# Optimization experiments

Measured on AMD Instinct MI355X. Metric: run time of the kernel, lower is better.

Reference implementation:

```python
import jax, jax.numpy as jnp
import numpy as np

B, P, D = 256, 128, 768        # batch, property slots per sample, encoder hidden dim
E = 64                          # num_properties (number of adapter heads)
H = 256                         # adapter_hidden_dim
H2 = H // 2
O = 2                           # output_dim
LN_EPS = 1e-5
RES_W_ADPT, RES_W_BASE = 0.7, 0.3


def setup_inputs() -> dict:
    key = jax.random.key(0)
    ks = jax.random.split(key, 12)
    hidden_states = jax.random.normal(ks[0], (B, P, D), dtype=jnp.float32)
    base_output = jax.random.normal(ks[1], (B, P, O), dtype=jnp.float32)
    properties = jax.random.randint(ks[2], (B, P), 0, E, dtype=jnp.int64)
    mask = (jax.random.uniform(ks[3], (B, P)) > 0.1).astype(jnp.float32)
    # Stacked per-head adapter parameters (LayerNorm + 3 Linears per head)
    ln_g = jnp.ones((E, D), dtype=jnp.float32)
    ln_b = jnp.zeros((E, D), dtype=jnp.float32)
    W1 = jax.random.normal(ks[4], (E, D, H), dtype=jnp.float32) * (1.0 / np.sqrt(D))
    b1 = jnp.zeros((E, H), dtype=jnp.float32)
    W2 = jax.random.normal(ks[5], (E, H, H2), dtype=jnp.float32) * (1.0 / np.sqrt(H))
    b2 = jnp.zeros((E, H2), dtype=jnp.float32)
    W3 = jax.random.normal(ks[6], (E, H2, O), dtype=jnp.float32) * 0.01  # init std=0.01 per source
    b3 = jnp.zeros((E, O), dtype=jnp.float32)
    return {
        "hidden_states": hidden_states, "base_output": base_output,
        "properties": properties, "mask": mask,
        "ln_g": ln_g, "ln_b": ln_b, "W1": W1, "b1": b1,
        "W2": W2, "b2": b2, "W3": W3, "b3": b3,
    }


def reference(hidden_states, base_output, properties, mask,
              ln_g, ln_b, W1, b1, W2, b2, W3, b3):
    b, p, d = hidden_states.shape
    o = W3.shape[-1]
    x = hidden_states.reshape(-1, d)                        # [N, D]
    # LayerNorm statistics are head-independent; only gamma/beta differ per head
    mu = jnp.mean(x, axis=-1, keepdims=True)
    var = jnp.mean((x - mu) ** 2, axis=-1, keepdims=True)
    xhat = (x - mu) * jax.lax.rsqrt(var + LN_EPS)           # [N, D]
    flat_p = properties.reshape(-1)                         # [N]
    flat_m = mask.reshape(-1)                               # [N]

    def body(acc, inp):
        idx, g, bt, w1, bb1, w2, bb2, w3, bb3 = inp
        h = jax.nn.relu((xhat * g + bt) @ w1 + bb1)         # [N, H]  (dropout = identity in eval)
        h = jax.nn.relu(h @ w2 + bb2)                       # [N, H2]
        out = h @ w3 + bb3                                  # [N, O]
        sel = (flat_p == idx) & (flat_m > 0)
        return jnp.where(sel[:, None], out, acc), None

    e = W1.shape[0]
    acc0 = jnp.zeros((b * p, o), dtype=x.dtype)
    acc, _ = jax.lax.scan(
        body, acc0,
        (jnp.arange(e), ln_g, ln_b, W1, b1, W2, b2, W3, b3))
    out = acc.reshape(b, p, o)
    out = RES_W_ADPT * out + RES_W_BASE * base_output       # use_residual=True
    return out * mask[..., None]
```

## Files before the change

kernel.cpp:

```cpp
#include <hip/hip_runtime.h>
#include <stdint.h>

typedef unsigned short u16;
typedef unsigned int   u32;

#define NTOK   32768
#define GD     768
#define GH     256
#define GH2    128
#define GE     64

typedef __bf16 bf16x8 __attribute__((ext_vector_type(8)));
typedef float  f32x4  __attribute__((ext_vector_type(4)));
union Frag { uint4 u; bf16x8 b; };

__device__ __forceinline__ float bf2f(u16 h) {
  union { u32 u; float f; } v; v.u = ((u32)h) << 16; return v.f;
}
__device__ __forceinline__ u16 f2bf(float f) {
  union { float f; u32 u; } v; v.f = f;
  u32 r = (v.u + 0x7fffu + ((v.u >> 16) & 1u)) >> 16;
  return (u16)r;
}

__device__ __forceinline__ void bar_lds() {
  asm volatile("s_waitcnt lgkmcnt(0)" ::: "memory");
  __builtin_amdgcn_sched_barrier(0);
  __builtin_amdgcn_s_barrier();
  __builtin_amdgcn_sched_barrier(0);
}

__device__ __forceinline__ int getProp(const int* p32, int t, int is64) {
  return is64 ? p32[2 * t] : p32[t];
}

static const size_t OFF_W1T  = 0;
static const size_t OFF_W2T  = 25165824;
static const size_t OFF_TOK  = 29360128;
static const size_t OFF_META = 29491200;

__global__ void setup_kernel(const int* __restrict__ prop, const float* __restrict__ mask,
                             u32* __restrict__ outz, int* __restrict__ counts2d,
                             int* __restrict__ cursors_p, int* __restrict__ flagp) {
  __shared__ int h[GE];
  __shared__ int vOr;
  const int b = blockIdx.x;
  const int tid = threadIdx.x;
  outz[b * 512 + tid] = 0u;
  outz[b * 512 + 256 + tid] = 0u;
  if (b < 4) cursors_p[b * 256 + tid] = 0;
  if (tid < GE) h[tid] = 0;
  if (tid == 0) vOr = 0;
  __syncthreads();
  int v = prop[2 * tid + 1] | prop[2 * (tid + 256) + 1];
  if (v) atomicOr(&vOr, 1);
  __syncthreads();
  const int is64 = (vOr == 0) ? 1 : 0;
  if (b == 0 && tid == 0) *flagp = is64;
  const int t = b * 256 + tid;
  if (mask[t] > 0.f) atomicAdd(&h[getProp(prop, t, is64)], 1);
  __syncthreads();
  if (tid < GE) counts2d[b * GE + tid] = h[tid];
}

__global__ void transpose_w1(const float* __restrict__ in, u16* __restrict__ out) {
  __shared__ u16 tl[64][260];
  const int bid = blockIdx.x;
  const int e  = bid / 12, r = bid % 12;
  const int d0 = (r / 4) * 256, h0 = (r % 4) * 64;
  const int tid = threadIdx.x;
  const size_t inMat = (size_t)e * GD * GH;
  const size_t outMat = (size_t)e * GH * GD;
  const int h_l = (tid & 15) * 4, d_l = tid >> 4;
#pragma unroll
  for (int dd = 0; dd < 16; ++dd) {
    const int d = d_l + dd * 16;
    float4 v = *(const float4*)(in + inMat + (size_t)(d0 + d) * GH + h0 + h_l);
    tl[h_l + 0][d] = f2bf(v.x);
    tl[h_l + 1][d] = f2bf(v.y);
    tl[h_l + 2][d] = f2bf(v.z);
    tl[h_l + 3][d] = f2bf(v.w);
  }
  __syncthreads();
  const int wv = tid >> 6, ln = tid & 63;
  const int d_glob = d0 + ln * 4;
  const size_t tbase = outMat + (size_t)(d_glob >> 5) * 8192 +
                       (size_t)((d_glob >> 3) & 3) * 2048 + (d_glob & 7);
#pragma unroll
  for (int hh = 0; hh < 16; ++hh) {
    const int h = wv * 16 + hh;
    *(uint2*)(out + tbase + (size_t)(h0 + h) * 8) = *(const uint2*)&tl[h][ln * 4];
  }
}

__global__ void transpose_w2(const float* __restrict__ in, u16* __restrict__ out) {
  __shared__ u16 tile[32][33];
  const int tilesPerMat = 32;
  const int e  = blockIdx.x / tilesPerMat;
  const int t  = blockIdx.x % tilesPerMat;
  const int tr = t / 4, tc = t % 4;
  const size_t mat = (size_t)e * GH * GH2;
  const int tx = threadIdx.x & 31, ty = threadIdx.x >> 5;
  const int r0 = tr * 32, c0 = tc * 32;
#pragma unroll
  for (int i = 0; i < 32; i += 8)
    tile[ty + i][tx] = f2bf(in[mat + (size_t)(r0 + ty + i) * GH2 + c0 + tx]);
  __syncthreads();
  const int k = r0 + tx;
  const size_t kbase = mat + (size_t)(k >> 5) * 4096 +
                       (size_t)((k >> 3) & 3) * 1024 + (k & 7);
#pragma unroll
  for (int i = 0; i < 32; i += 8)
    out[kbase + (size_t)(c0 + ty + i) * 8] = tile[tx][ty + i];
}

__global__ void scan_kernel(const int* __restrict__ counts2d, int* __restrict__ offsets,
                            int* __restrict__ tileHead, int* __restrict__ tileRow,
                            int* __restrict__ nTilesPtr) {
  __shared__ int part[4][GE];
  const int tid = threadIdx.x;
  const int e = tid & 63, q = tid >> 6;
  int c = 0;
  for (int b = q * 32; b < q * 32 + 32; ++b) c += counts2d[b * GE + e];
  part[q][e] = c;
  __syncthreads();
  if (tid < GE) {
    const int ct = part[0][e] + part[1][e] + part[2][e] + part[3][e];
    int inc = ct;
#pragma unroll
    for (int d = 1; d < 64; d <<= 1) { int n = __shfl_up(inc, d); if (e >= d) inc += n; }
    const int off = inc - ct;
    offsets[e] = off;
    if (e == 63) offsets[64] = inc;
    int ntile = (ct + 63) >> 6;
    int inct = ntile;
#pragma unroll
    for (int d = 1; d < 64; d <<= 1) { int n = __shfl_up(inct, d); if (e >= d) inct += n; }
    const int tb = inct - ntile;
    for (int j = 0; j < ntile; ++j) { tileHead[tb + j] = e; tileRow[tb + j] = off + j * 64; }
    if (e == 63) *nTilesPtr = inct;
  }
}

__global__ void scatter_kernel(const int* __restrict__ prop, const float* __restrict__ mask,
                               const int* __restrict__ offsets, int* __restrict__ cursors_p,
                               int* __restrict__ tokenIds, const int* __restrict__ flag) {
  __shared__ int h[GE];
  __shared__ int basebin[GE];
  const int tid = threadIdx.x;
  const int t = blockIdx.x * 256 + tid;
  if (tid < GE) h[tid] = 0;
  __syncthreads();
  int p = -1, rank = 0;
  if (mask[t] > 0.f) {
    p = getProp(prop, t, *flag);
    rank = atomicAdd(&h[p], 1);
  }
  __syncthreads();
  if (tid < GE && h[tid] > 0) basebin[tid] = atomicAdd(&cursors_p[tid * 16], h[tid]);
  __syncthreads();
  if (p >= 0) tokenIds[offsets[p] + basebin[p] + rank] = t;
}

__global__ __launch_bounds__(256, 2) void adapter_gemm(
    const float* __restrict__ hs, const u16* __restrict__ w1t, const u16* __restrict__ w2t,
    const float* __restrict__ lng, const float* __restrict__ lnb,
    const float* __restrict__ b1, const float* __restrict__ b2,
    const float* __restrict__ w3, const float* __restrict__ b3,
    const float* __restrict__ base, const float* __restrict__ mask,
    const int* __restrict__ tokenIds, const int* __restrict__ offsets,
    const int* __restrict__ tileHead, const int* __restrict__ tileRow,
    const int* __restrict__ nTilesPtr, float* __restrict__ outp) {
  __shared__ union LU {
    u16 A[3][2048];
    u16 h[17408];
  } uni;
  __shared__ float sBias1[256];
  __shared__ float sBias2[128];
  __shared__ float sW3[2][128];
  __shared__ float sB3[2];
  __shared__ int   sTok[64];
  __shared__ __align__(16) float sGam[GD];
  __shared__ __align__(16) float sBet[GD];
  __shared__ float sMu[64];
  __shared__ float sRstd[64];

  const int tid  = threadIdx.x;
  const int wv   = tid >> 6;
  const int l15  = tid & 15;
  const int quad = (tid & 63) >> 4;
  const f32x4 vzero = {0.f, 0.f, 0.f, 0.f};
  const int nt = *nTilesPtr;
  const int qq = nt >> 3, rr = nt & 7;

  for (int i = blockIdx.x; i < nt; i += gridDim.x) {
    const int x = i & 7, s = i >> 3;
    const int tile = (x < rr ? x * (qq + 1) : rr * (qq + 1) + (x - rr) * qq) + s;

    __syncthreads();
    const int e  = tileHead[tile];
    const int rs = tileRow[tile];
    const int nRows = min(64, offsets[e + 1] - rs);

    if (tid < 64) sTok[tid] = tokenIds[rs + min(tid, nRows - 1)];
    sBias1[tid] = b1[e * GH + tid];
    if (tid < 128) sBias2[tid] = b2[e * GH2 + tid];
    { const int k = tid >> 1, o = tid & 1; sW3[o][k] = w3[e * GH2 * 2 + k * 2 + o]; }
    if (tid < 2) sB3[tid] = b3[e * 2 + tid];
    __syncthreads();

    const u16* w1e = w1t + (size_t)e * GH * GD;
    const u16* w2e = w2t + (size_t)e * GH2 * GH;

    if (tid < 192) {
      *(float4*)&sGam[tid * 4] = *(const float4*)(lng + (size_t)e * GD + tid * 4);
      *(float4*)&sBet[tid * 4] = *(const float4*)(lnb + (size_t)e * GD + tid * 4);
    }

    const int r0  = tid >> 3;
    const int klo = (tid & 7) * 4;
    const int kgrp = klo >> 3, kin = klo & 7;
    const float* xA = hs + (size_t)sTok[r0] * GD + klo;
    const float* xB = hs + (size_t)sTok[r0 + 32] * GD + klo;

    Frag fbE[4], fbO[4];
#define LOAD_FB(DST, KT) do {                                                   \
    const u16* _g = w1e + (KT) * 8192 + quad * 2048;                            \
    DST[0].u = *(const uint4*)(_g + (size_t)(wv * 64 +  0 + l15) * 8);          \
    DST[1].u = *(const uint4*)(_g + (size_t)(wv * 64 + 16 + l15) * 8);          \
    DST[2].u = *(const uint4*)(_g + (size_t)(wv * 64 + 32 + l15) * 8);          \
    DST[3].u = *(const uint4*)(_g + (size_t)(wv * 64 + 48 + l15) * 8);          \
  } while (0)

#define ISSUE_PA(D, KT) do {                                                    \
    pA[D][0] = *(const float4*)(xA + (KT) * 32);                                \
    pA[D][1] = *(const float4*)(xB + (KT) * 32);                                \
  } while (0)

    float4 pA[3][2];
    ISSUE_PA(0, 0);
    ISSUE_PA(1, 1);
    ISSUE_PA(2, 2);
    LOAD_FB(fbE, 0);
    LOAD_FB(fbO, 1);
    __builtin_amdgcn_sched_barrier(0);

#pragma unroll 2
    for (int pass = 0; pass < 4; ++pass) {
      const int row = pass * 16 + (tid >> 4);
      const int l16 = tid & 15;
      const float* xp = hs + (size_t)sTok[row] * GD + l16 * 4;
      float sm = 0.f, sq = 0.f;
#pragma unroll
      for (int c = 0; c < 12; ++c) {
        float4 u = *(const float4*)(xp + c * 64);
        sm += u.x + u.y + u.z + u.w;
        sq += u.x*u.x + u.y*u.y + u.z*u.z + u.w*u.w;
      }
#pragma unroll
      for (int d = 1; d < 16; d <<= 1) { sm += __shfl_xor(sm, d); sq += __shfl_xor(sq, d); }
      if (l16 == 0) {
        const float mu = sm * (1.f / 768.f);
        sMu[row] = mu;
        sRstd[row] = rsqrtf(sq * (1.f / 768.f) - mu * mu + 1e-5f);
      }
    }
    bar_lds();

    const float muA = sMu[r0],      rsA = sRstd[r0];
    const float muB = sMu[r0 + 32], rsB = sRstd[r0 + 32];

#define XFORM_WRITE(PAR, D, K0) do {                                            \
    const float4 gv = *(const float4*)&sGam[(K0) + klo];                        \
    const float4 bv = *(const float4*)&sBet[(K0) + klo];                        \
    const float4 va = pA[D][0], vb = pA[D][1];                                  \
    uint2 oa, ob;                                                               \
    oa.x = (u32)f2bf((va.x - muA) * rsA * gv.x + bv.x)                          \
         | ((u32)f2bf((va.y - muA) * rsA * gv.y + bv.y) << 16);                 \
    oa.y = (u32)f2bf((va.z - muA) * rsA * gv.z + bv.z)                          \
         | ((u32)f2bf((va.w - muA) * rsA * gv.w + bv.w) << 16);                 \
    ob.x = (u32)f2bf((vb.x - muB) * rsB * gv.x + bv.x)                          \
         | ((u32)f2bf((vb.y - muB) * rsB * gv.y + bv.y) << 16);                 \
    ob.y = (u32)f2bf((vb.z - muB) * rsB * gv.z + bv.z)                          \
         | ((u32)f2bf((vb.w - muB) * rsB * gv.w + bv.w) << 16);                 \
    *(uint2*)&uni.A[PAR][kgrp * 512 + r0 * 8 + kin] = oa;                       \
    *(uint2*)&uni.A[PAR][kgrp * 512 + (r0 + 32) * 8 + kin] = ob;                \
  } while (0)

    XFORM_WRITE(0, 0, 0);
    XFORM_WRITE(1, 1, 32);
    bar_lds();

    f32x4 acc1[4][4];
#pragma unroll
    for (int f = 0; f < 4; ++f)
#pragma unroll
      for (int g = 0; g < 4; ++g) acc1[f][g] = vzero;

#pragma unroll
    for (int kt = 0; kt < 24; ++kt) {
      Frag fa[4];
#pragma unroll
      for (int f = 0; f < 4; ++f)
        fa[f].u = *(const uint4*)&uni.A[kt % 3][quad * 512 + (f * 16 + l15) * 8];
      if ((kt & 1) == 0) {
#pragma unroll
        for (int f = 0; f < 4; ++f)
#pragma unroll
          for (int g = 0; g < 4; ++g)
            acc1[f][g] = __builtin_amdgcn_mfma_f32_16x16x32_bf16(fa[f].b, fbE[g].b, acc1[f][g], 0, 0, 0);
        if (kt + 2 < 24) LOAD_FB(fbE, kt + 2);
      } else {
#pragma unroll
        for (int f = 0; f < 4; ++f)
#pragma unroll
          for (int g = 0; g < 4; ++g)
            acc1[f][g] = __builtin_amdgcn_mfma_f32_16x16x32_bf16(fa[f].b, fbO[g].b, acc1[f][g], 0, 0, 0);
        if (kt + 2 < 24) LOAD_FB(fbO, kt + 2);
      }
      if (kt + 2 < 24)
        XFORM_WRITE((kt + 2) % 3, (kt + 2) % 3, (kt + 2) * 32);
      if (kt + 3 < 24)
        ISSUE_PA((kt + 3) % 3, kt + 3);
      bar_lds();
    }
    bar_lds();

    Frag bW2[8][2];
#pragma unroll
    for (int kt = 0; kt < 8; ++kt)
#pragma unroll
      for (int g = 0; g < 2; ++g)
        bW2[kt][g].u = *(const uint4*)(w2e + kt * 4096 + quad * 1024 +
                                       (size_t)(wv * 32 + g * 16 + l15) * 8);

#pragma unroll
    for (int f = 0; f < 4; ++f)
#pragma unroll
      for (int g = 0; g < 4; ++g) {
        const int col = wv * 64 + g * 16 + l15;
        const float bias = sBias1[col];
#pragma unroll
        for (int r = 0; r < 4; ++r) {
          const int row = f * 16 + quad * 4 + r;
          uni.h[row * 264 + col] = f2bf(fmaxf(acc1[f][g][r] + bias, 0.f));
        }
      }
    bar_lds();

    f32x4 acc2[4][2];
#pragma unroll
    for (int f = 0; f < 4; ++f)
#pragma unroll
      for (int g = 0; g < 2; ++g) acc2[f][g] = vzero;

#pragma unroll
    for (int kt = 0; kt < 8; ++kt) {
      Frag fa2[4];
#pragma unroll
      for (int f = 0; f < 4; ++f)
        fa2[f].u = *(const uint4*)&uni.h[(f * 16 + l15) * 264 + kt * 32 + quad * 8];
#pragma unroll
      for (int f = 0; f < 4; ++f)
#pragma unroll
        for (int g = 0; g < 2; ++g)
          acc2[f][g] = __builtin_amdgcn_mfma_f32_16x16x32_bf16(fa2[f].b, bW2[kt][g].b, acc2[f][g], 0, 0, 0);
    }
    bar_lds();

#pragma unroll
    for (int f = 0; f < 4; ++f)
#pragma unroll
      for (int g = 0; g < 2; ++g) {
        const int col = wv * 32 + g * 16 + l15;
        const float bias = sBias2[col];
#pragma unroll
        for (int r = 0; r < 4; ++r) {
          const int row = f * 16 + quad * 4 + r;
          uni.h[row * 130 + col] = f2bf(fmaxf(acc2[f][g][r] + bias, 0.f));
        }
      }
    bar_lds();

    const int m = tid >> 1, o = tid & 1;
    if (m < nRows) {
      float a = sB3[o];
      const u16* h2row = &uni.h[m * 130];
#pragma unroll 16
      for (int k = 0; k < 128; ++k) a += bf2f(h2row[k]) * sW3[o][k];
      const int t = sTok[m];
      const float mk = mask[t];
      const float bs = base[t * 2 + o];
      outp[t * 2 + o] = (0.7f * a + 0.3f * bs) * mk;
    }
  }
#undef XFORM_WRITE
#undef ISSUE_PA
#undef LOAD_FB
}

extern "C" void kernel_launch(void* const* d_in, const int* in_sizes, int n_in,
                              void* d_out, int out_size, void* d_ws, size_t ws_size,
                              hipStream_t stream) {
  const float* hs   = (const float*)d_in[0];
  const float* base = (const float*)d_in[1];
  const int*   prop = (const int*)d_in[2];
  const float* mask = (const float*)d_in[3];
  const float* lng  = (const float*)d_in[4];
  const float* lnb  = (const float*)d_in[5];
  const float* W1   = (const float*)d_in[6];
  const float* b1   = (const float*)d_in[7];
  const float* W2   = (const float*)d_in[8];
  const float* b2   = (const float*)d_in[9];
  const float* W3   = (const float*)d_in[10];
  const float* b3   = (const float*)d_in[11];

  char* ws = (char*)d_ws;
  u16* w1t  = (u16*)(ws + OFF_W1T);
  u16* w2t  = (u16*)(ws + OFF_W2T);
  int* tok  = (int*)(ws + OFF_TOK);
  int* meta = (int*)(ws + OFF_META);
  int* counts2d  = meta;
  int* offsets   = meta + 8192;
  int* tileHead  = meta + 8320;
  int* tileRow   = meta + 9344;
  int* nTiles    = meta + 10368;
  int* propFlag  = meta + 10369;
  int* cursors_p = meta + 10432;

  setup_kernel<<<128, 256, 0, stream>>>(prop, mask, (u32*)d_out, counts2d,
                                        cursors_p, propFlag);
  transpose_w1<<<768, 256, 0, stream>>>(W1, w1t);
  transpose_w2<<<64 * 32, 256, 0, stream>>>(W2, w2t);
  scan_kernel<<<1, 256, 0, stream>>>(counts2d, offsets, tileHead, tileRow, nTiles);
  scatter_kernel<<<NTOK / 256, 256, 0, stream>>>(prop, mask, offsets, cursors_p, tok, propFlag);
  adapter_gemm<<<640, 256, 0, stream>>>(hs, w1t, w2t, lng, lnb, b1, b2, W3, b3,
                                        base, mask, tok, offsets, tileHead, tileRow,
                                        nTiles, (float*)d_out);
}
```

Baseline: 250.9 us.

## Fuse weight transposes, widen scan, quad-buffer A tile with fewer barriers

Merges the W1 and W2 bf16 transpose kernels into a single launch, and widens the count-reduction scan to 1024 threads. In the GEMM main loop, the A-tile LDS buffer grows from three to four slots so a barrier is needed only every other k-step. The W3 dot product also uses four independent accumulators. Together these aim to cut launch overhead and barrier stalls, at the cost of more LDS per block and more reliance on getting the buffer-reuse distance right.

```diff
diff --git a/kernel.cpp b/kernel.cpp
--- a/kernel.cpp
+++ b/kernel.cpp
@@ -63,69 +63,74 @@
   if (tid < GE) counts2d[b * GE + tid] = h[tid];
 }
 
-__global__ void transpose_w1(const float* __restrict__ in, u16* __restrict__ out) {
+__global__ void transpose_fused(const float* __restrict__ in1, u16* __restrict__ out1,
+                                const float* __restrict__ in2, u16* __restrict__ out2) {
   __shared__ u16 tl[64][260];
-  const int bid = blockIdx.x;
-  const int e  = bid / 12, r = bid % 12;
-  const int d0 = (r / 4) * 256, h0 = (r % 4) * 64;
   const int tid = threadIdx.x;
-  const size_t inMat = (size_t)e * GD * GH;
-  const size_t outMat = (size_t)e * GH * GD;
-  const int h_l = (tid & 15) * 4, d_l = tid >> 4;
-#pragma unroll
-  for (int dd = 0; dd < 16; ++dd) {
-    const int d = d_l + dd * 16;
-    float4 v = *(const float4*)(in + inMat + (size_t)(d0 + d) * GH + h0 + h_l);
-    tl[h_l + 0][d] = f2bf(v.x);
-    tl[h_l + 1][d] = f2bf(v.y);
-    tl[h_l + 2][d] = f2bf(v.z);
-    tl[h_l + 3][d] = f2bf(v.w);
+  if (blockIdx.x < 768) {
+    const int bid = blockIdx.x;
+    const int e  = bid / 12, r = bid % 12;
+    const int d0 = (r / 4) * 256, h0 = (r % 4) * 64;
+    const size_t inMat = (size_t)e * GD * GH;
+    const size_t outMat = (size_t)e * GH * GD;
+    const int h_l = (tid & 15) * 4, d_l = tid >> 4;
+#pragma unroll
+    for (int dd = 0; dd < 16; ++dd) {
+      const int d = d_l + dd * 16;
+      float4 v = *(const float4*)(in1 + inMat + (size_t)(d0 + d) * GH + h0 + h_l);
+      tl[h_l + 0][d] = f2bf(v.x);
+      tl[h_l + 1][d] = f2bf(v.y);
+      tl[h_l + 2][d] = f2bf(v.z);
+      tl[h_l + 3][d] = f2bf(v.w);
+    }
+    __syncthreads();
+    const int wv = tid >> 6, ln = tid & 63;
+    const int d_glob = d0 + ln * 4;
+    const size_t tbase = outMat + (size_t)(d_glob >> 5) * 8192 +
+                         (size_t)((d_glob >> 3) & 3) * 2048 + (d_glob & 7);
+#pragma unroll
+    for (int hh = 0; hh < 16; ++hh) {
+      const int h = wv * 16 + hh;
+      *(uint2*)(out1 + tbase + (size_t)(h0 + h) * 8) = *(const uint2*)&tl[h][ln * 4];
+    }
+  } else {
+    u16 (*tile)[33] = (u16(*)[33])tl;
+    const int bid = blockIdx.x - 768;
+    const int tilesPerMat = 32;
+    const int e  = bid / tilesPerMat;
+    const int t  = bid % tilesPerMat;
+    const int tr = t / 4, tc = t % 4;
+    const size_t mat = (size_t)e * GH * GH2;
+    const int tx = tid & 31, ty = tid >> 5;
+    const int r0 = tr * 32, c0 = tc * 32;
+#pragma unroll
+    for (int i = 0; i < 32; i += 8)
+      tile[ty + i][tx] = f2bf(in2[mat + (size_t)(r0 + ty + i) * GH2 + c0 + tx]);
+    __syncthreads();
+    const int k = r0 + tx;
+    const size_t kbase = mat + (size_t)(k >> 5) * 4096 +
+                         (size_t)((k >> 3) & 3) * 1024 + (k & 7);
+#pragma unroll
+    for (int i = 0; i < 32; i += 8)
+      out2[kbase + (size_t)(c0 + ty + i) * 8] = tile[tx][ty + i];
   }
-  __syncthreads();
-  const int wv = tid >> 6, ln = tid & 63;
-  const int d_glob = d0 + ln * 4;
-  const size_t tbase = outMat + (size_t)(d_glob >> 5) * 8192 +
-                       (size_t)((d_glob >> 3) & 3) * 2048 + (d_glob & 7);
-#pragma unroll
-  for (int hh = 0; hh < 16; ++hh) {
-    const int h = wv * 16 + hh;
-    *(uint2*)(out + tbase + (size_t)(h0 + h) * 8) = *(const uint2*)&tl[h][ln * 4];
-  }
-}
-
-__global__ void transpose_w2(const float* __restrict__ in, u16* __restrict__ out) {
-  __shared__ u16 tile[32][33];
-  const int tilesPerMat = 32;
-  const int e  = blockIdx.x / tilesPerMat;
-  const int t  = blockIdx.x % tilesPerMat;
-  const int tr = t / 4, tc = t % 4;
-  const size_t mat = (size_t)e * GH * GH2;
-  const int tx = threadIdx.x & 31, ty = threadIdx.x >> 5;
-  const int r0 = tr * 32, c0 = tc * 32;
-#pragma unroll
-  for (int i = 0; i < 32; i += 8)
-    tile[ty + i][tx] = f2bf(in[mat + (size_t)(r0 + ty + i) * GH2 + c0 + tx]);
-  __syncthreads();
-  const int k = r0 + tx;
-  const size_t kbase = mat + (size_t)(k >> 5) * 4096 +
-                       (size_t)((k >> 3) & 3) * 1024 + (k & 7);
-#pragma unroll
-  for (int i = 0; i < 32; i += 8)
-    out[kbase + (size_t)(c0 + ty + i) * 8] = tile[tx][ty + i];
 }
 
 __global__ void scan_kernel(const int* __restrict__ counts2d, int* __restrict__ offsets,
                             int* __restrict__ tileHead, int* __restrict__ tileRow,
                             int* __restrict__ nTilesPtr) {
-  __shared__ int part[4][GE];
+  __shared__ int part[16][GE];
   const int tid = threadIdx.x;
   const int e = tid & 63, q = tid >> 6;
   int c = 0;
-  for (int b = q * 32; b < q * 32 + 32; ++b) c += counts2d[b * GE + e];
+#pragma unroll
+  for (int b = 0; b < 8; ++b) c += counts2d[(q * 8 + b) * GE + e];
   part[q][e] = c;
   __syncthreads();
   if (tid < GE) {
-    const int ct = part[0][e] + part[1][e] + part[2][e] + part[3][e];
+    int ct = 0;
+#pragma unroll
+    for (int q2 = 0; q2 < 16; ++q2) ct += part[q2][e];
     int inc = ct;
 #pragma unroll
     for (int d = 1; d < 64; d <<= 1) { int n = __shfl_up(inc, d); if (e >= d) inc += n; }
@@ -172,7 +177,7 @@
     const int* __restrict__ tileHead, const int* __restrict__ tileRow,
     const int* __restrict__ nTilesPtr, float* __restrict__ outp) {
   __shared__ union LU {
-    u16 A[3][2048];
+    u16 A[4][2048];
     u16 h[17408];
   } uni;
   __shared__ float sBias1[256];
@@ -302,7 +307,7 @@
       Frag fa[4];
 #pragma unroll
       for (int f = 0; f < 4; ++f)
-        fa[f].u = *(const uint4*)&uni.A[kt % 3][quad * 512 + (f * 16 + l15) * 8];
+        fa[f].u = *(const uint4*)&uni.A[kt & 3][quad * 512 + (f * 16 + l15) * 8];
       if ((kt & 1) == 0) {
 #pragma unroll
         for (int f = 0; f < 4; ++f)
@@ -319,12 +324,11 @@
         if (kt + 2 < 24) LOAD_FB(fbO, kt + 2);
       }
       if (kt + 2 < 24)
-        XFORM_WRITE((kt + 2) % 3, (kt + 2) % 3, (kt + 2) * 32);
+        XFORM_WRITE((kt + 2) & 3, (kt + 2) % 3, (kt + 2) * 32);
       if (kt + 3 < 24)
         ISSUE_PA((kt + 3) % 3, kt + 3);
-      bar_lds();
-    }
-    bar_lds();
+      if (kt & 1) bar_lds();
+    }
 
     Frag bW2[8][2];
 #pragma unroll
@@ -384,10 +388,17 @@
 
     const int m = tid >> 1, o = tid & 1;
     if (m < nRows) {
-      float a = sB3[o];
       const u16* h2row = &uni.h[m * 130];
-#pragma unroll 16
-      for (int k = 0; k < 128; ++k) a += bf2f(h2row[k]) * sW3[o][k];
+      const float* w3r = sW3[o];
+      float a0 = 0.f, a1 = 0.f, a2 = 0.f, a3 = 0.f;
+#pragma unroll 8
+      for (int k = 0; k < 128; k += 4) {
+        a0 += bf2f(h2row[k + 0]) * w3r[k + 0];
+        a1 += bf2f(h2row[k + 1]) * w3r[k + 1];
+        a2 += bf2f(h2row[k + 2]) * w3r[k + 2];
+        a3 += bf2f(h2row[k + 3]) * w3r[k + 3];
+      }
+      const float a = sB3[o] + ((a0 + a1) + (a2 + a3));
       const int t = sTok[m];
       const float mk = mask[t];
       const float bs = base[t * 2 + o];
@@ -430,9 +441,8 @@
 
   setup_kernel<<<128, 256, 0, stream>>>(prop, mask, (u32*)d_out, counts2d,
                                         cursors_p, propFlag);
-  transpose_w1<<<768, 256, 0, stream>>>(W1, w1t);
-  transpose_w2<<<64 * 32, 256, 0, stream>>>(W2, w2t);
-  scan_kernel<<<1, 256, 0, stream>>>(counts2d, offsets, tileHead, tileRow, nTiles);
+  transpose_fused<<<768 + 2048, 256, 0, stream>>>(W1, w1t, W2, w2t);
+  scan_kernel<<<1, 1024, 0, stream>>>(counts2d, offsets, tileHead, tileRow, nTiles);
   scatter_kernel<<<NTOK / 256, 256, 0, stream>>>(prop, mask, offsets, cursors_p, tok, propFlag);
   adapter_gemm<<<640, 256, 0, stream>>>(hs, w1t, w2t, lng, lnb, b1, b2, W3, b3,
                                         base, mask, tok, offsets, tileHead, tileRow,
```

Result: no change. 254.7 us (+1.5%).
